# Optimization experiments

Hardware: AMD Instinct MI355X
Metric: run time of the kernel (lower is better)

The kernel has to match this reference:

```python
import jax, jax.numpy as jnp
import numpy as np
import math

C, NH, HD, L, P, FFN = 256, 8, 32, 1, 4, 512
H_BEV, W_BEV = 200, 100
NQ, BS, NV = 1000, 4, H_BEV * W_BEV
EPS = 1e-5


def _ln(x, g, b):
    m = x.mean(-1, keepdims=True)
    v = ((x - m) ** 2).mean(-1, keepdims=True)
    return (x - m) / jnp.sqrt(v + EPS) * g + b


def _mha(x, qpos, in_w, in_b, ow, ob):
    # nn.MultiheadAttention self-attention; key_pos = query_pos (shapes match)
    q = x + qpos
    k = x + qpos
    v = x
    wq, wk, wv = jnp.split(in_w, 3, axis=0)
    bq, bk, bv = jnp.split(in_b, 3, axis=0)
    bs, nq, _ = x.shape
    qh = (q @ wq.T + bq).reshape(bs, nq, NH, HD)
    kh = (k @ wk.T + bk).reshape(bs, nq, NH, HD)
    vh = (v @ wv.T + bv).reshape(bs, nq, NH, HD)
    scores = jnp.einsum('bqhd,bkhd->bhqk', qh, kh) / jnp.sqrt(jnp.float32(HD))
    attn = jax.nn.softmax(scores, axis=-1)
    out = jnp.einsum('bhqk,bkhd->bqhd', attn, vh).reshape(bs, nq, C)
    return out @ ow.T + ob


def _msdeform(x, qpos, value, ref, spatial_shapes, so_w, so_b, aw_w, aw_b, vp_w, vp_b, op_w, op_b):
    # Multi-scale deformable attention (single level), bilinear sampling with
    # align_corners=False convention and zero padding, as in the CUDA kernel.
    bs, nq, _ = x.shape
    q = x + qpos
    v = (value @ vp_w.T + vp_b).reshape(bs, NV, NH, HD).transpose(0, 2, 1, 3)  # [bs,nh,nv,hd]
    off = (q @ so_w.T + so_b).reshape(bs, nq, NH, L, P, 2)
    aw = jax.nn.softmax((q @ aw_w.T + aw_b).reshape(bs, nq, NH, L * P), axis=-1)
    aw = aw.reshape(bs, nq, NH, L, P)
    norm = jnp.stack([spatial_shapes[:, 1], spatial_shapes[:, 0]], -1).astype(jnp.float32)  # [L,2] = (W,H)
    loc = ref[:, :, None, :, None, :] + off / norm[None, None, None, :, None, :]  # [bs,nq,nh,L,P,2]
    loc = loc[:, :, :, 0]  # single level -> [bs,nq,nh,P,2]
    awp = aw[:, :, :, 0]   # [bs,nq,nh,P]
    x_im = loc[..., 0] * W_BEV - 0.5
    y_im = loc[..., 1] * H_BEV - 0.5
    x0 = jnp.floor(x_im)
    y0 = jnp.floor(y_im)
    lx = x_im - x0
    ly = y_im - y0
    x0i = x0.astype(jnp.int32)
    y0i = y0.astype(jnp.int32)
    acc = jnp.zeros((bs, NH, nq, P, HD), jnp.float32)
    for dy in (0, 1):
        for dx in (0, 1):
            xi = x0i + dx
            yi = y0i + dy
            w = (lx if dx else 1.0 - lx) * (ly if dy else 1.0 - ly)  # [bs,nq,nh,P]
            ok = ((xi >= 0) & (xi < W_BEV) & (yi >= 0) & (yi < H_BEV)).astype(jnp.float32)
            idx = jnp.clip(yi, 0, H_BEV - 1) * W_BEV + jnp.clip(xi, 0, W_BEV - 1)
            idx_t = idx.transpose(0, 2, 1, 3).reshape(bs, NH, nq * P)
            g = jnp.take_along_axis(v, idx_t[..., None], axis=2).reshape(bs, NH, nq, P, HD)
            acc = acc + g * (w * ok).transpose(0, 2, 1, 3)[..., None]
    out = (acc * awp.transpose(0, 2, 1, 3)[..., None]).sum(3)  # [bs,nh,nq,hd]
    out = out.transpose(0, 2, 1, 3).reshape(bs, nq, C)
    return out @ op_w.T + op_b


def setup_inputs() -> dict:
    key = jax.random.key(0)
    ks = jax.random.split(key, 24)
    f32 = jnp.float32

    def w(k, shp):
        fan = shp[-1]
        return (jax.random.normal(k, shp, f32) * (1.0 / np.sqrt(fan))).astype(f32)

    # sampling_offsets bias per _reset_parameters (radial grid init)
    thetas = np.arange(NH, dtype=np.float32) * (2.0 * math.pi / NH)
    grid = np.stack([np.cos(thetas), np.sin(thetas)], -1)
    grid = grid / np.abs(grid).max(-1, keepdims=True)
    grid = np.tile(grid[:, None, None, :], (1, L, P, 1))
    for i in range(P):
        grid[:, :, i, :] *= i + 1
    so_b = jnp.asarray(grid.reshape(-1), f32)

    return {
        'query': jax.random.normal(ks[0], (NQ, BS, C), f32),
        'value': jax.random.normal(ks[1], (NV, BS, C), f32),
        'query_pos': jax.random.normal(ks[2], (NQ, BS, C), f32),
        'reference_points': jax.random.uniform(ks[3], (BS, NQ, L, 2), f32),
        'spatial_shapes': jnp.array([[H_BEV, W_BEV]], jnp.int32),
        'level_start_index': jnp.zeros((L,), jnp.int32),
        'in_proj_w': w(ks[4], (3 * C, C)),
        'in_proj_b': jnp.zeros((3 * C,), f32),
        'mha_ow': w(ks[5], (C, C)),
        'mha_ob': jnp.zeros((C,), f32),
        'so_w': w(ks[6], (NH * L * P * 2, C)) * 0.01,
        'so_b': so_b,
        'aw_w': w(ks[7], (NH * L * P, C)) * 0.01,
        'aw_b': jnp.zeros((NH * L * P,), f32),
        'vp_w': w(ks[8], (C, C)),
        'vp_b': jnp.zeros((C,), f32),
        'op_w': w(ks[9], (C, C)),
        'op_b': jnp.zeros((C,), f32),
        'ffn_w1': w(ks[10], (FFN, C)),
        'ffn_b1': jnp.zeros((FFN,), f32),
        'ffn_w2': w(ks[11], (C, FFN)),
        'ffn_b2': jnp.zeros((C,), f32),
        'ln1_g': jnp.ones((C,), f32), 'ln1_b': jnp.zeros((C,), f32),
        'ln2_g': jnp.ones((C,), f32), 'ln2_b': jnp.zeros((C,), f32),
        'ln3_g': jnp.ones((C,), f32), 'ln3_b': jnp.zeros((C,), f32),
    }


def reference(query, value, query_pos, reference_points, spatial_shapes, level_start_index,
              in_proj_w, in_proj_b, mha_ow, mha_ob, so_w, so_b, aw_w, aw_b,
              vp_w, vp_b, op_w, op_b, ffn_w1, ffn_b1, ffn_w2, ffn_b2,
              ln1_g, ln1_b, ln2_g, ln2_b, ln3_g, ln3_b):
    # batch_first=False: (seq, bs, C) -> (bs, seq, C)
    x = query.transpose(1, 0, 2)
    val = value.transpose(1, 0, 2)
    qpos = query_pos.transpose(1, 0, 2)
    # self_attn -> norm (residual inside attn wrapper; dropout=0 in eval)
    x = _ln(x + _mha(x, qpos, in_proj_w, in_proj_b, mha_ow, mha_ob), ln1_g, ln1_b)
    # cross_attn (MSDeformAttn) -> norm
    x = _ln(x + _msdeform(x, qpos, val, reference_points, spatial_shapes,
                          so_w, so_b, aw_w, aw_b, vp_w, vp_b, op_w, op_b), ln2_g, ln2_b)
    # ffn -> norm
    h = jax.nn.relu(x @ ffn_w1.T + ffn_b1) @ ffn_w2.T + ffn_b2
    x = _ln(x + h, ln3_g, ln3_b)
    return x.transpose(1, 0, 2)
```

## Files before the change

kernel.cpp:

```cpp
#include <hip/hip_runtime.h>
#include <hip/hip_bf16.h>
#include <cmath>

#define BS   4
#define NQ   1000
#define CDIM 256
#define NH   8
#define HD   32
#define NVAL 20000
#define FFND 512
#define PN   4
#define WBEV 100
#define HBEV 200
#define TK   64

typedef __bf16 v8bf __attribute__((ext_vector_type(8)));
typedef __bf16 v2bf __attribute__((ext_vector_type(2)));
typedef float  v4f  __attribute__((ext_vector_type(4)));

__device__ __forceinline__ void gload_lds16(const void* g, void* l) {
    __builtin_amdgcn_global_load_lds(
        (const __attribute__((address_space(1))) unsigned int*)g,
        (__attribute__((address_space(3))) unsigned int*)l, 16, 0, 0);
}

__device__ __forceinline__ void vgemm64_block(
    int vb, const float* __restrict__ value, const __bf16* __restrict__ Wv,
    const float* __restrict__ bv, __bf16* __restrict__ vpj, char* smem)
{
    __bf16* As = (__bf16*)smem;
    __bf16* Bs = (__bf16*)(smem + 8192);
    int tid = threadIdx.x;
    int wave = tid >> 6, lane = tid & 63, quad = lane >> 4, n16 = lane & 15;
    int bm = vb * 64;
    int wm = (wave & 1) * 32, wn = (wave >> 1) * 128;
    v4f acc[2][8] = {};

    for (int k0 = 0; k0 < 256; k0 += 64) {
        float4 fa[2][2];
        #pragma unroll
        for (int i = 0; i < 2; i++) {
            int e = i * 256 + tid;
            int r = e >> 3, c = (e & 7) ^ (r & 7);
            const float* p = value + (long)(bm + r) * 256 + k0 + c * 8;
            fa[i][0] = *(const float4*)p;
            fa[i][1] = *(const float4*)(p + 4);
        }
        __syncthreads();
        #pragma unroll
        for (int i = 0; i < 2; i++) {
            int e = i * 256 + tid;
            v8bf v;
            v[0] = (__bf16)fa[i][0].x; v[1] = (__bf16)fa[i][0].y;
            v[2] = (__bf16)fa[i][0].z; v[3] = (__bf16)fa[i][0].w;
            v[4] = (__bf16)fa[i][1].x; v[5] = (__bf16)fa[i][1].y;
            v[6] = (__bf16)fa[i][1].z; v[7] = (__bf16)fa[i][1].w;
            *(v8bf*)(As + e * 8) = v;
        }
        #pragma unroll
        for (int i = 0; i < 8; i++) {
            int e = i * 256 + tid;
            int r = e >> 3, c = (e & 7) ^ (r & 7);
            gload_lds16(Wv + (long)r * 256 + k0 + c * 8, Bs + e * 8);
        }
        __syncthreads();
        #pragma unroll
        for (int s = 0; s < 2; s++) {
            v8bf af[2], bfr[8];
            #pragma unroll
            for (int mi = 0; mi < 2; mi++) {
                int row = wm + mi * 16 + n16;
                af[mi] = *(v8bf*)&As[row * 64 + (((quad + s * 4) ^ (row & 7))) * 8];
            }
            #pragma unroll
            for (int nj = 0; nj < 8; nj++) {
                int row = wn + nj * 16 + n16;
                bfr[nj] = *(v8bf*)&Bs[row * 64 + (((quad + s * 4) ^ (row & 7))) * 8];
            }
            #pragma unroll
            for (int mi = 0; mi < 2; mi++)
                #pragma unroll
                for (int nj = 0; nj < 8; nj++)
                    acc[mi][nj] = __builtin_amdgcn_mfma_f32_16x16x32_bf16(af[mi], bfr[nj], acc[mi][nj], 0, 0, 0);
        }
    }
    #pragma unroll
    for (int mi = 0; mi < 2; mi++) {
        #pragma unroll
        for (int r = 0; r < 4; r++) {
            int m = bm + wm + mi * 16 + quad * 4 + r;
            #pragma unroll
            for (int nj = 0; nj < 8; nj++) {
                int nn = wn + nj * 16 + n16;
                vpj[(long)m * 256 + nn] = (__bf16)(acc[mi][nj][r] + bv[nn]);
            }
        }
    }
}

__global__ __launch_bounds__(256) void prep_all_kernel(
    const float* __restrict__ query, const float* __restrict__ qpos,
    const float* __restrict__ in_w, const float* __restrict__ mha_ow,
    const float* __restrict__ vp_w, const float* __restrict__ op_w,
    const float* __restrict__ ffn_w1, const float* __restrict__ ffn_w2,
    const float* __restrict__ so_w, const float* __restrict__ aw_w,
    const float* __restrict__ so_b, const float* __restrict__ aw_b,
    float* __restrict__ x, float* __restrict__ qpos_t,
    __bf16* __restrict__ x_bf, __bf16* __restrict__ xq_bf,
    __bf16* __restrict__ wb, __bf16* __restrict__ wsmall,
    float* __restrict__ bsmall)
{
    int blk = blockIdx.x, tid = threadIdx.x;
    if (blk < 640) {
        long e = ((long)blk * 256 + tid) * 4;
        const float* src; long off;
        if      (e < 196608) { src = in_w;   off = e; }
        else if (e < 262144) { src = mha_ow; off = e - 196608; }
        else if (e < 327680) { src = vp_w;   off = e - 262144; }
        else if (e < 393216) { src = op_w;   off = e - 327680; }
        else if (e < 524288) { src = ffn_w1; off = e - 393216; }
        else                 { src = ffn_w2; off = e - 524288; }
        float4 v = *(const float4*)(src + off);
        __bf16* d = wb + e;
        d[0] = (__bf16)v.x; d[1] = (__bf16)v.y; d[2] = (__bf16)v.z; d[3] = (__bf16)v.w;
    } else if (blk < 4640) {
        int qb = blk - 640;
        int q = qb / BS, b = qb % BS;
        float qv = query[(q * BS + b) * CDIM + tid];
        float pv = qpos [(q * BS + b) * CDIM + tid];
        int o = (b * NQ + q) * CDIM + tid;
        x[o] = qv; qpos_t[o] = pv;
        x_bf[o] = (__bf16)qv; xq_bf[o] = (__bf16)(qv + pv);
    } else if (blk < 4672) {
        long e = ((long)(blk - 4640) * 256 + tid) * 4;
        int row = (int)(e >> 8), col = (int)(e & 255);
        float4 v = {0.f, 0.f, 0.f, 0.f};
        if (row < 64)      v = *(const float4*)(so_w + row * 256 + col);
        else if (row < 96) v = *(const float4*)(aw_w + (row - 64) * 256 + col);
        __bf16* d = wsmall + e;
        d[0] = (__bf16)v.x; d[1] = (__bf16)v.y; d[2] = (__bf16)v.z; d[3] = (__bf16)v.w;
    } else {
        if (tid < 128) bsmall[tid] = tid < 64 ? so_b[tid] : (tid < 96 ? aw_b[tid - 64] : 0.f);
    }
}

__global__ __launch_bounds__(256) void qkvv_kernel(
    const __bf16* __restrict__ xq, const __bf16* __restrict__ xv,
    const __bf16* __restrict__ W, const float* __restrict__ bias,
    __bf16* __restrict__ qk, __bf16* __restrict__ vh,
    const float* __restrict__ value, const __bf16* __restrict__ Wv,
    const float* __restrict__ bv, __bf16* __restrict__ vpj, int voff)
{
    __shared__ __align__(16) char smem[40960];
    int tid = threadIdx.x;
    if ((int)blockIdx.x >= 756) {
        vgemm64_block(blockIdx.x - 756 + voff, value, Wv, bv, vpj, smem);
        return;
    }
    int blk = blockIdx.x;
    int bn = (blk % 12) * 64, bm = (blk / 12) * 64;
    __bf16* As = (__bf16*)smem;
    __bf16* Bs = (__bf16*)(smem + 8192);
    const __bf16* A = (bn < 512) ? xq : xv;
    int wave = tid >> 6, lane = tid & 63, quad = lane >> 4, n16 = lane & 15;
    int wm = (wave & 1) * 32, wn = (wave >> 1) * 32;
    v4f acc[2][2] = {};

    for (int k0 = 0; k0 < 256; k0 += 64) {
        __syncthreads();
        #pragma unroll
        for (int i = 0; i < 2; i++) {
            int e = i * 256 + tid;
            int r = e >> 3, c = (e & 7) ^ (r & 7);
            int row = bm + r; if (row > BS * NQ - 1) row = BS * NQ - 1;
            gload_lds16(A + (long)row * 256 + k0 + c * 8, As + e * 8);
        }
        #pragma unroll
        for (int i = 0; i < 2; i++) {
            int e = i * 256 + tid;
            int r = e >> 3, c = (e & 7) ^ (r & 7);
            gload_lds16(W + (long)(bn + r) * 256 + k0 + c * 8, Bs + e * 8);
        }
        __syncthreads();
        #pragma unroll
        for (int s = 0; s < 2; s++) {
            v8bf af[2], bfr[2];
            #pragma unroll
            for (int mi = 0; mi < 2; mi++) {
                int row = wm + mi * 16 + n16;
                af[mi] = *(v8bf*)&As[row * 64 + (((quad + s * 4) ^ (row & 7))) * 8];
            }
            #pragma unroll
            for (int nj = 0; nj < 2; nj++) {
                int row = wn + nj * 16 + n16;
                bfr[nj] = *(v8bf*)&Bs[row * 64 + (((quad + s * 4) ^ (row & 7))) * 8];
            }
            #pragma unroll
            for (int mi = 0; mi < 2; mi++)
                #pragma unroll
                for (int nj = 0; nj < 2; nj++)
                    acc[mi][nj] = __builtin_amdgcn_mfma_f32_16x16x32_bf16(af[mi], bfr[nj], acc[mi][nj], 0, 0, 0);
        }
    }

    #pragma unroll
    for (int mi = 0; mi < 2; mi++) {
        #pragma unroll
        for (int r = 0; r < 4; r++) {
            int m = bm + wm + mi * 16 + quad * 4 + r;
            if (m >= BS * NQ) continue;
            #pragma unroll
            for (int nj = 0; nj < 2; nj++) {
                int nn = bn + wn + nj * 16 + n16;
                float v = acc[mi][nj][r] + bias[nn];
                if (nn < 512) qk[(long)m * 512 + nn] = (__bf16)v;
                else          vh[(long)m * 256 + (nn - 512)] = (__bf16)v;
            }
        }
    }
}

__global__ __launch_bounds__(256) void fattnv_kernel(
    const __bf16* __restrict__ qk, const __bf16* __restrict__ vh,
    __bf16* __restrict__ aout,
    const float* __restrict__ value, const __bf16* __restrict__ Wv,
    const float* __restrict__ bv, __bf16* __restrict__ vpj, int voff)
{
    __shared__ __align__(16) char smem[40960];
    int tid = threadIdx.x;
    if ((int)blockIdx.x >= 512) {
        vgemm64_block(blockIdx.x - 512 + voff, value, Wv, bv, vpj, smem);
        return;
    }
    int fb = blockIdx.x;
    int qt = fb & 15, h = (fb >> 4) & 7, b = fb >> 7;
    __bf16* Ks = (__bf16*)smem;
    __bf16* Vt = (__bf16*)(smem + 10240);
    __bf16* Pl = (__bf16*)(smem + 19456);
    int wave = tid >> 6, lane = tid & 63, quad = lane >> 4, n = lane & 15;
    int q0 = qt * 64 + wave * 16;
    const float scale = 0.17677669529663687f;
    const float M0 = 8.0f;

    int qrow = q0 + n; if (qrow > NQ - 1) qrow = NQ - 1;
    v8bf aq = *(const v8bf*)(qk + (long)(b * NQ + qrow) * 512 + h * HD + quad * 8);

    v4f o0 = {}, o1 = {};
    float lp[4] = {0.f, 0.f, 0.f, 0.f};

    int sv = tid >> 7;
    int t2 = tid & 127;
    int key = t2 & 63;
    int d16 = (t2 >> 6) * 16;

    v8bf stg0, stg1;
    auto loadtile = [&](int k0) {
        int krow = k0 + key; if (krow > NQ - 1) krow = NQ - 1;
        const __bf16* p = sv ? (vh + (long)(b * NQ + krow) * CDIM + h * HD + d16)
                             : (qk + (long)(b * NQ + krow) * 512 + 256 + h * HD + d16);
        stg0 = *(const v8bf*)p;
        stg1 = *(const v8bf*)(p + 8);
    };

    loadtile(0);
    int pb = 0;
    for (int k0 = 0; k0 < NQ; k0 += TK) {
        if (sv == 0) {
            *(v8bf*)&Ks[(pb * 64 + key) * 40 + d16]     = stg0;
            *(v8bf*)&Ks[(pb * 64 + key) * 40 + d16 + 8] = stg1;
        } else {
            #pragma unroll
            for (int j = 0; j < 8; j++) {
                Vt[(pb * 32 + d16 + j) * 72 + key]            = stg0[j];
                Vt[(pb * 32 + d16 + 8 + j) * 72 + (key ^ 16)] = stg1[j];
            }
        }
        if (k0 + TK < NQ) loadtile(k0 + TK);
        __syncthreads();

        v8bf bk0 = *(v8bf*)&Ks[(pb * 64 +      n) * 40 + quad * 8];
        v8bf bk1 = *(v8bf*)&Ks[(pb * 64 + 16 + n) * 40 + quad * 8];
        v8bf bk2 = *(v8bf*)&Ks[(pb * 64 + 32 + n) * 40 + quad * 8];
        v8bf bk3 = *(v8bf*)&Ks[(pb * 64 + 48 + n) * 40 + quad * 8];
        v4f z = {};
        v4f S0 = __builtin_amdgcn_mfma_f32_16x16x32_bf16(aq, bk0, z, 0, 0, 0);
        v4f S1 = __builtin_amdgcn_mfma_f32_16x16x32_bf16(aq, bk1, z, 0, 0, 0);
        v4f S2 = __builtin_amdgcn_mfma_f32_16x16x32_bf16(aq, bk2, z, 0, 0, 0);
        v4f S3 = __builtin_amdgcn_mfma_f32_16x16x32_bf16(aq, bk3, z, 0, 0, 0);

        bool last = (k0 + TK > NQ);
        float p0[4], p1[4], p2[4], p3[4];
        #pragma unroll
        for (int r = 0; r < 4; r++) {
            p0[r] = __expf(fmaf(S0[r], scale, -M0));
            p1[r] = __expf(fmaf(S1[r], scale, -M0));
            p2[r] = __expf(fmaf(S2[r], scale, -M0));
            p3[r] = __expf(fmaf(S3[r], scale, -M0));
            if (last) {
                if (k0 + 32 + n >= NQ) p2[r] = 0.f;
                if (k0 + 48 + n >= NQ) p3[r] = 0.f;
            }
            lp[r] += p0[r] + p1[r] + p2[r] + p3[r];
        }
        #pragma unroll
        for (int r = 0; r < 4; r++) {
            __bf16* pp = &Pl[(wave * 16 + quad * 4 + r) * 72];
            pp[n]      = (__bf16)p0[r];
            pp[16 + n] = (__bf16)p1[r];
            pp[32 + n] = (__bf16)p2[r];
            pp[48 + n] = (__bf16)p3[r];
        }
        asm volatile("s_waitcnt lgkmcnt(0)" ::: "memory");
        v8bf ap0 = *(v8bf*)&Pl[(wave * 16 + n) * 72 + quad * 8];
        v8bf ap1 = *(v8bf*)&Pl[(wave * 16 + n) * 72 + 32 + quad * 8];
        int swz = ((n >> 3) & 1) << 4;
        int c0 = (quad * 8) ^ swz;
        int c1 = (32 + quad * 8) ^ swz;
        v8bf bv00 = *(v8bf*)&Vt[(pb * 32 +      n) * 72 + c0];
        v8bf bv01 = *(v8bf*)&Vt[(pb * 32 +      n) * 72 + c1];
        v8bf bv10 = *(v8bf*)&Vt[(pb * 32 + 16 + n) * 72 + c0];
        v8bf bv11 = *(v8bf*)&Vt[(pb * 32 + 16 + n) * 72 + c1];
        o0 = __builtin_amdgcn_mfma_f32_16x16x32_bf16(ap0, bv00, o0, 0, 0, 0);
        o0 = __builtin_amdgcn_mfma_f32_16x16x32_bf16(ap1, bv01, o0, 0, 0, 0);
        o1 = __builtin_amdgcn_mfma_f32_16x16x32_bf16(ap0, bv10, o1, 0, 0, 0);
        o1 = __builtin_amdgcn_mfma_f32_16x16x32_bf16(ap1, bv11, o1, 0, 0, 0);
        pb ^= 1;
    }

    #pragma unroll
    for (int r = 0; r < 4; r++) {
        float l = lp[r];
        #pragma unroll
        for (int off = 1; off < 16; off <<= 1) l += __shfl_xor(l, off, 16);
        int q = q0 + quad * 4 + r;
        if (q < NQ) {
            float invl = 1.0f / l;
            __bf16* op = aout + ((long)(b * NQ + q) * CDIM + h * HD);
            op[n]      = (__bf16)(o0[r] * invl);
            op[16 + n] = (__bf16)(o1[r] * invl);
        }
    }
}

__global__ __launch_bounds__(256) void gln1s_kernel(
    const __bf16* __restrict__ A, const __bf16* __restrict__ W,
    const float* __restrict__ bias, const float* __restrict__ res,
    const float* __restrict__ g, const float* __restrict__ beta,
    const float* __restrict__ qpos_t,
    const __bf16* __restrict__ Wsm, const float* __restrict__ bsm,
    float* __restrict__ outf, float* __restrict__ soawO,
    const float* __restrict__ value, const __bf16* __restrict__ Wv,
    const float* __restrict__ bv, __bf16* __restrict__ vpj, int voff)
{
    __shared__ __align__(16) char smem[43776];
    int tid = threadIdx.x;
    if ((int)blockIdx.x >= 250) {
        vgemm64_block(blockIdx.x - 250 + voff, value, Wv, bv, vpj, smem);
        return;
    }
    __bf16* As  = (__bf16*)smem;
    __bf16* Bs  = (__bf16*)(smem + 2048);
    __bf16* Axq = (__bf16*)(smem + 34816);
    float* redS = (float*)(smem + 43264);
    float* redQ = redS + 64;
    int bm = blockIdx.x * 16;
    int wave = tid >> 6, lane = tid & 63, quad = lane >> 4, n16 = lane & 15;
    int wn = wave * 64;
    v4f acc[4] = {};

    for (int k0 = 0; k0 < 256; k0 += 64) {
        __syncthreads();
        if (tid < 128) {
            int e = tid;
            int r = e >> 3, c = (e & 7) ^ (r & 7);
            gload_lds16(A + (long)(bm + r) * 256 + k0 + c * 8, As + e * 8);
        }
        #pragma unroll
        for (int i = 0; i < 8; i++) {
            int e = i * 256 + tid;
            int r = e >> 3, c = (e & 7) ^ (r & 7);
            gload_lds16(W + (long)r * 256 + k0 + c * 8, Bs + e * 8);
        }
        __syncthreads();
        #pragma unroll
        for (int s = 0; s < 2; s++) {
            v8bf af = *(v8bf*)&As[n16 * 64 + (((quad + s * 4) ^ (n16 & 7))) * 8];
            #pragma unroll
            for (int nj = 0; nj < 4; nj++) {
                int row = wn + nj * 16 + n16;
                v8bf bfr = *(v8bf*)&Bs[row * 64 + (((quad + s * 4) ^ (row & 7))) * 8];
                acc[nj] = __builtin_amdgcn_mfma_f32_16x16x32_bf16(af, bfr, acc[nj], 0, 0, 0);
            }
        }
    }

    float y[4][4], s1[4] = {}, s2[4] = {};
    #pragma unroll
    for (int r = 0; r < 4; r++) {
        int m = bm + quad * 4 + r;
        #pragma unroll
        for (int nj = 0; nj < 4; nj++) {
            int nn = wn + nj * 16 + n16;
            float v = acc[nj][r] + bias[nn] + res[(long)m * 256 + nn];
            y[r][nj] = v;
            s1[r] += v; s2[r] += v * v;
        }
    }
    #pragma unroll
    for (int r = 0; r < 4; r++) {
        #pragma unroll
        for (int off = 1; off < 16; off <<= 1) {
            s1[r] += __shfl_xor(s1[r], off, 16);
            s2[r] += __shfl_xor(s2[r], off, 16);
        }
    }
    if (n16 == 0) {
        #pragma unroll
        for (int r = 0; r < 4; r++) {
            redS[wave * 16 + quad * 4 + r] = s1[r];
            redQ[wave * 16 + quad * 4 + r] = s2[r];
        }
    }
    __syncthreads();
    #pragma unroll
    for (int r = 0; r < 4; r++) {
        int mr = quad * 4 + r;
        float ts = redS[mr] + redS[16 + mr] + redS[32 + mr] + redS[48 + mr];
        float tq = redQ[mr] + redQ[16 + mr] + redQ[32 + mr] + redQ[48 + mr];
        float mean = ts * (1.0f / 256.0f);
        float var = tq * (1.0f / 256.0f) - mean * mean;
        float rinv = rsqrtf(var + 1e-5f);
        int m = bm + mr;
        #pragma unroll
        for (int nj = 0; nj < 4; nj++) {
            int nn = wn + nj * 16 + n16;
            float o = (y[r][nj] - mean) * rinv * g[nn] + beta[nn];
            outf[(long)m * 256 + nn] = o;
            Axq[mr * 264 + nn] = (__bf16)(o + qpos_t[(long)m * 256 + nn]);
        }
    }
    __syncthreads();
    if (wave < 3) {
        v4f sacc[2] = {};
        #pragma unroll
        for (int k0 = 0; k0 < 256; k0 += 32) {
            v8bf af = *(v8bf*)&Axq[n16 * 264 + k0 + quad * 8];
            #pragma unroll
            for (int t = 0; t < 2; t++) {
                int col = wave * 32 + t * 16 + n16;
                v8bf bw = *(const v8bf*)(Wsm + (long)col * 256 + k0 + quad * 8);
                sacc[t] = __builtin_amdgcn_mfma_f32_16x16x32_bf16(af, bw, sacc[t], 0, 0, 0);
            }
        }
        #pragma unroll
        for (int t = 0; t < 2; t++)
            #pragma unroll
            for (int r = 0; r < 4; r++) {
                int mm = bm + quad * 4 + r;
                int col = wave * 32 + t * 16 + n16;
                soawO[(long)mm * 96 + col] = sacc[t][r] + bsm[col];
            }
    }
}

__global__ __launch_bounds__(256) void msds_kernel(
    const __bf16* __restrict__ vproj, const float* __restrict__ soaw,
    const float* __restrict__ refp, __bf16* __restrict__ out)
{
    int t = threadIdx.x;
    int bq = blockIdx.x * 2 + (t >> 7);
    int b = bq / NQ; int q = bq % NQ;
    int t2 = t & 127;
    int h = t2 >> 4;
    int d0 = (t2 & 15) * 2;
    float rx = refp[(b * NQ + q) * 2 + 0];
    float ry = refp[(b * NQ + q) * 2 + 1];
    const float* rowp = soaw + (long)(b * NQ + q) * 96;
    const float* offp = rowp + h * 8;
    const float* awp  = rowp + 64 + h * 4;
    float a0 = awp[0], a1 = awp[1], a2 = awp[2], a3 = awp[3];
    float m = fmaxf(fmaxf(a0, a1), fmaxf(a2, a3));
    float e0 = __expf(a0 - m), e1 = __expf(a1 - m), e2 = __expf(a2 - m), e3 = __expf(a3 - m);
    float invs = 1.0f / (e0 + e1 + e2 + e3);
    float accA = 0.f, accB = 0.f;
    #pragma unroll
    for (int p = 0; p < PN; p++) {
        float ew = (p == 0 ? e0 : p == 1 ? e1 : p == 2 ? e2 : e3) * invs;
        float xim = rx * (float)WBEV + offp[p * 2 + 0] - 0.5f;
        float yim = ry * (float)HBEV + offp[p * 2 + 1] - 0.5f;
        float x0f = floorf(xim), y0f = floorf(yim);
        float lx = xim - x0f, ly = yim - y0f;
        int x0 = (int)x0f, y0 = (int)y0f;
        float gA = 0.f, gB = 0.f;
        #pragma unroll
        for (int dy = 0; dy < 2; dy++) {
            #pragma unroll
            for (int dx = 0; dx < 2; dx++) {
                int xi = x0 + dx, yi = y0 + dy;
                float w = (dx ? lx : 1.f - lx) * (dy ? ly : 1.f - ly);
                bool ok = (xi >= 0 && xi < WBEV && yi >= 0 && yi < HBEV);
                int xc = min(max(xi, 0), WBEV - 1);
                int yc = min(max(yi, 0), HBEV - 1);
                int idx = yc * WBEV + xc;
                v2bf gv = *(const v2bf*)(vproj + ((long)(idx * BS + b)) * CDIM + h * HD + d0);
                float wk = (ok ? w : 0.f);
                gA += wk * (float)gv[0];
                gB += wk * (float)gv[1];
            }
        }
        accA += ew * gA;
        accB += ew * gB;
    }
    v2bf o2; o2[0] = (__bf16)accA; o2[1] = (__bf16)accB;
    *(v2bf*)(out + (long)(b * NQ + q) * CDIM + h * HD + d0) = o2;
}

__global__ __launch_bounds__(256) void gtail_kernel(
    const __bf16* __restrict__ A, const __bf16* __restrict__ Wop,
    const float* __restrict__ opb, const float* __restrict__ res,
    const float* __restrict__ g2, const float* __restrict__ b2ln,
    const __bf16* __restrict__ W1, const float* __restrict__ b1,
    const __bf16* __restrict__ W2, const float* __restrict__ bff2,
    const float* __restrict__ g3, const float* __restrict__ b3ln,
    float* __restrict__ outf)
{
    __shared__ __align__(16) char smem[59904];
    __bf16* As  = (__bf16*)smem;
    __bf16* Bs  = (__bf16*)(smem + 2048);
    __bf16* As2 = (__bf16*)(smem + 34816);
    __bf16* h1s = (__bf16*)(smem + 43008);
    float* redS = (float*)(smem + 59392);
    float* redQ = (float*)(smem + 59648);
    int tid = threadIdx.x;
    int bm = blockIdx.x * 16;
    int wave = tid >> 6, lane = tid & 63, quad = lane >> 4, n16 = lane & 15;
    int wn = wave * 64;

    v4f acc[4] = {};
    for (int k0 = 0; k0 < 256; k0 += 64) {
        __syncthreads();
        if (tid < 128) {
            int e = tid;
            int r = e >> 3, c = (e & 7) ^ (r & 7);
            gload_lds16(A + (long)(bm + r) * 256 + k0 + c * 8, As + e * 8);
        }
        #pragma unroll
        for (int i = 0; i < 8; i++) {
            int e = i * 256 + tid;
            int r = e >> 3, c = (e & 7) ^ (r & 7);
            gload_lds16(Wop + (long)r * 256 + k0 + c * 8, Bs + e * 8);
        }
        __syncthreads();
        #pragma unroll
        for (int s = 0; s < 2; s++) {
            v8bf af = *(v8bf*)&As[n16 * 64 + (((quad + s * 4) ^ (n16 & 7))) * 8];
            #pragma unroll
            for (int nj = 0; nj < 4; nj++) {
                int row = wn + nj * 16 + n16;
                v8bf bfr = *(v8bf*)&Bs[row * 64 + (((quad + s * 4) ^ (row & 7))) * 8];
                acc[nj] = __builtin_amdgcn_mfma_f32_16x16x32_bf16(af, bfr, acc[nj], 0, 0, 0);
            }
        }
    }
    float yv[4][4], s1[4] = {}, s2[4] = {};
    #pragma unroll
    for (int r = 0; r < 4; r++) {
        int m = bm + quad * 4 + r;
        #pragma unroll
        for (int nj = 0; nj < 4; nj++) {
            int nn = wn + nj * 16 + n16;
            float v = acc[nj][r] + opb[nn] + res[(long)m * 256 + nn];
            yv[r][nj] = v;
            s1[r] += v; s2[r] += v * v;
        }
    }
    #pragma unroll
    for (int r = 0; r < 4; r++) {
        #pragma unroll
        for (int off = 1; off < 16; off <<= 1) {
            s1[r] += __shfl_xor(s1[r], off, 16);
            s2[r] += __shfl_xor(s2[r], off, 16);
        }
    }
    if (n16 == 0) {
        #pragma unroll
        for (int r = 0; r < 4; r++) {
            redS[wave * 16 + quad * 4 + r] = s1[r];
            redQ[wave * 16 + quad * 4 + r] = s2[r];
        }
    }
    __syncthreads();
    #pragma unroll
    for (int r = 0; r < 4; r++) {
        int mr = quad * 4 + r;
        float ts = redS[mr] + redS[16 + mr] + redS[32 + mr] + redS[48 + mr];
        float tq = redQ[mr] + redQ[16 + mr] + redQ[32 + mr] + redQ[48 + mr];
        float mean = ts * (1.0f / 256.0f);
        float var = tq * (1.0f / 256.0f) - mean * mean;
        float rinv = rsqrtf(var + 1e-5f);
        #pragma unroll
        for (int nj = 0; nj < 4; nj++) {
            int nn = wn + nj * 16 + n16;
            float o = (yv[r][nj] - mean) * rinv * g2[nn] + b2ln[nn];
            yv[r][nj] = o;
            int c = nn & 63;
            As2[wave * 1024 + mr * 64 + ((((c >> 3)) ^ (mr & 7)) << 3) + (c & 7)] = (__bf16)o;
        }
    }

    #pragma unroll 1
    for (int H = 0; H < 2; H++) {
        v4f accB[4] = {};
        for (int k0 = 0; k0 < 256; k0 += 64) {
            __syncthreads();
            #pragma unroll
            for (int i = 0; i < 8; i++) {
                int e = i * 256 + tid;
                int r = e >> 3, c = (e & 7) ^ (r & 7);
                gload_lds16(W1 + (long)(H * 256 + r) * 256 + k0 + c * 8, Bs + e * 8);
            }
            __syncthreads();
            int kc = k0 >> 6;
            #pragma unroll
            for (int s = 0; s < 2; s++) {
                v8bf af = *(v8bf*)&As2[kc * 1024 + n16 * 64 + (((quad + s * 4) ^ (n16 & 7))) * 8];
                #pragma unroll
                for (int nj = 0; nj < 4; nj++) {
                    int row = wn + nj * 16 + n16;
                    v8bf bfr = *(v8bf*)&Bs[row * 64 + (((quad + s * 4) ^ (row & 7))) * 8];
                    accB[nj] = __builtin_amdgcn_mfma_f32_16x16x32_bf16(af, bfr, accB[nj], 0, 0, 0);
                }
            }
        }
        #pragma unroll
        for (int r = 0; r < 4; r++) {
            int mr = quad * 4 + r;
            #pragma unroll
            for (int nj = 0; nj < 4; nj++) {
                int col = H * 256 + wn + nj * 16 + n16;
                float v = accB[nj][r] + b1[col];
                v = fmaxf(v, 0.f);
                int kc = col >> 6, c = col & 63;
                h1s[kc * 1024 + mr * 64 + ((((c >> 3)) ^ (mr & 7)) << 3) + (c & 7)] = (__bf16)v;
            }
        }
    }

    v4f acc3[4] = {};
    for (int k0 = 0; k0 < 512; k0 += 64) {
        __syncthreads();
        #pragma unroll
        for (int i = 0; i < 8; i++) {
            int e = i * 256 + tid;
            int r = e >> 3, c = (e & 7) ^ (r & 7);
            gload_lds16(W2 + (long)r * 512 + k0 + c * 8, Bs + e * 8);
        }
        __syncthreads();
        int kc = k0 >> 6;
        #pragma unroll
        for (int s = 0; s < 2; s++) {
            v8bf af = *(v8bf*)&h1s[kc * 1024 + n16 * 64 + (((quad + s * 4) ^ (n16 & 7))) * 8];
            #pragma unroll
            for (int nj = 0; nj < 4; nj++) {
                int row = wn + nj * 16 + n16;
                v8bf bfr = *(v8bf*)&Bs[row * 64 + (((quad + s * 4) ^ (row & 7))) * 8];
                acc3[nj] = __builtin_amdgcn_mfma_f32_16x16x32_bf16(af, bfr, acc3[nj], 0, 0, 0);
            }
        }
    }
    float y3[4][4], t1[4] = {}, t2[4] = {};
    #pragma unroll
    for (int r = 0; r < 4; r++) {
        #pragma unroll
        for (int nj = 0; nj < 4; nj++) {
            int nn = wn + nj * 16 + n16;
            float v = acc3[nj][r] + bff2[nn] + yv[r][nj];
            y3[r][nj] = v;
            t1[r] += v; t2[r] += v * v;
        }
    }
    #pragma unroll
    for (int r = 0; r < 4; r++) {
        #pragma unroll
        for (int off = 1; off < 16; off <<= 1) {
            t1[r] += __shfl_xor(t1[r], off, 16);
            t2[r] += __shfl_xor(t2[r], off, 16);
        }
    }
    __syncthreads();
    if (n16 == 0) {
        #pragma unroll
        for (int r = 0; r < 4; r++) {
            redS[wave * 16 + quad * 4 + r] = t1[r];
            redQ[wave * 16 + quad * 4 + r] = t2[r];
        }
    }
    __syncthreads();
    #pragma unroll
    for (int r = 0; r < 4; r++) {
        int mr = quad * 4 + r;
        float ts = redS[mr] + redS[16 + mr] + redS[32 + mr] + redS[48 + mr];
        float tq = redQ[mr] + redQ[16 + mr] + redQ[32 + mr] + redQ[48 + mr];
        float mean = ts * (1.0f / 256.0f);
        float var = tq * (1.0f / 256.0f) - mean * mean;
        float rinv = rsqrtf(var + 1e-5f);
        int m = bm + mr;
        int b = m / NQ, q = m - b * NQ;
        #pragma unroll
        for (int nj = 0; nj < 4; nj++) {
            int nn = wn + nj * 16 + n16;
            float o = (y3[r][nj] - mean) * rinv * g3[nn] + b3ln[nn];
            outf[(long)(q * BS + b) * 256 + nn] = o;
        }
    }
}

extern "C" void kernel_launch(void* const* d_in, const int* in_sizes, int n_in,
                              void* d_out, int out_size, void* d_ws, size_t ws_size,
                              hipStream_t stream) {
    const float* query = (const float*)d_in[0];
    const float* value = (const float*)d_in[1];
    const float* qpos  = (const float*)d_in[2];
    const float* refp  = (const float*)d_in[3];
    const float* in_w  = (const float*)d_in[6];
    const float* in_b  = (const float*)d_in[7];
    const float* mha_ow = (const float*)d_in[8];
    const float* mha_ob = (const float*)d_in[9];
    const float* so_w  = (const float*)d_in[10];
    const float* so_b  = (const float*)d_in[11];
    const float* aw_w  = (const float*)d_in[12];
    const float* aw_b  = (const float*)d_in[13];
    const float* vp_w  = (const float*)d_in[14];
    const float* vp_b  = (const float*)d_in[15];
    const float* op_w  = (const float*)d_in[16];
    const float* op_b  = (const float*)d_in[17];
    const float* ffn_w1 = (const float*)d_in[18];
    const float* ffn_b1 = (const float*)d_in[19];
    const float* ffn_w2 = (const float*)d_in[20];
    const float* ffn_b2 = (const float*)d_in[21];
    const float* ln1_g = (const float*)d_in[22];
    const float* ln1_b = (const float*)d_in[23];
    const float* ln2_g = (const float*)d_in[24];
    const float* ln2_b = (const float*)d_in[25];
    const float* ln3_g = (const float*)d_in[26];
    const float* ln3_b = (const float*)d_in[27];
    float* out = (float*)d_out;

    const long NTOK = (long)BS * NQ * CDIM;

    float* x      = (float*)d_ws;
    float* qpos_t = x + NTOK;
    float* x1     = qpos_t + NTOK;
    float* x2     = x1 + NTOK;
    float* soaw   = x2 + NTOK;
    float* bsmall = soaw + (long)BS * NQ * 96;
    __bf16* x_bf   = (__bf16*)(bsmall + 128);
    __bf16* xq_bf  = x_bf + NTOK;
    __bf16* qk_bf  = xq_bf + NTOK;
    __bf16* vh_bf  = qk_bf + 2 * NTOK;
    __bf16* aA_bf  = vh_bf + NTOK;
    __bf16* x2_bf  = aA_bf + NTOK;
    __bf16* h1_bf  = x2_bf + NTOK;
    __bf16* vpj_bf = h1_bf + 2 * NTOK;
    __bf16* wb     = vpj_bf + (long)BS * NVAL * CDIM;
    __bf16* inw_b  = wb;
    __bf16* mow_b  = wb + 196608;
    __bf16* vpw_b  = wb + 262144;
    __bf16* opw_b  = wb + 327680;
    __bf16* fw1_b  = wb + 393216;
    __bf16* fw2_b  = wb + 524288;
    __bf16* wsmall = wb + 655360;

    dim3 blk(256);

    prep_all_kernel<<<4673, blk, 0, stream>>>(
        query, qpos, in_w, mha_ow, vp_w, op_w, ffn_w1, ffn_w2,
        so_w, aw_w, so_b, aw_b,
        x, qpos_t, x_bf, xq_bf, wb, wsmall, bsmall);

    qkvv_kernel<<<1173, blk, 0, stream>>>(xq_bf, x_bf, inw_b, in_b, qk_bf, vh_bf,
                                          value, vpw_b, vp_b, vpj_bf, 0);

    fattnv_kernel<<<929, blk, 0, stream>>>(qk_bf, vh_bf, aA_bf,
                                           value, vpw_b, vp_b, vpj_bf, 417);

    gln1s_kernel<<<666, blk, 0, stream>>>(
        aA_bf, mow_b, mha_ob, x, ln1_g, ln1_b, qpos_t, wsmall, bsmall,
        x1, soaw, value, vpw_b, vp_b, vpj_bf, 834);

    msds_kernel<<<2000, blk, 0, stream>>>(vpj_bf, soaw, refp, aA_bf);

    gtail_kernel<<<250, blk, 0, stream>>>(
        aA_bf, opw_b, op_b, x1, ln2_g, ln2_b,
        fw1_b, ffn_b1, fw2_b, ffn_b2, ln3_g, ln3_b, out);
}
```

Before: 270.5 us.

## Split value projection into standalone kernel and widen FFN tail blocks to 512 threads

Before this change, the value-projection GEMM blocks were spread across the qkv, attention and LN1 kernels to overlap with them. They now run as one dedicated vgemm kernel with 1250 blocks, and the host kernels shrink their LDS to match their own needs. Separately, the FFN tail kernel goes to 512 threads (8 waves, each covering 32 columns), which gives more parallelism per 16-row block in its 250-block grid. The cost is losing the overlap of the value GEMM with the latency-bound attention work, plus one extra launch.

```diff
diff --git a/kernel.cpp b/kernel.cpp
--- a/kernel.cpp
+++ b/kernel.cpp
@@ -24,15 +24,16 @@
         (__attribute__((address_space(3))) unsigned int*)l, 16, 0, 0);
 }
 
-__device__ __forceinline__ void vgemm64_block(
-    int vb, const float* __restrict__ value, const __bf16* __restrict__ Wv,
-    const float* __restrict__ bv, __bf16* __restrict__ vpj, char* smem)
+__global__ __launch_bounds__(256) void vgemm_kernel(
+    const float* __restrict__ value, const __bf16* __restrict__ Wv,
+    const float* __restrict__ bv, __bf16* __restrict__ vpj)
 {
+    __shared__ __align__(16) char smem[40960];
     __bf16* As = (__bf16*)smem;
     __bf16* Bs = (__bf16*)(smem + 8192);
     int tid = threadIdx.x;
     int wave = tid >> 6, lane = tid & 63, quad = lane >> 4, n16 = lane & 15;
-    int bm = vb * 64;
+    int bm = blockIdx.x * 64;
     int wm = (wave & 1) * 32, wn = (wave >> 1) * 128;
     v4f acc[2][8] = {};
 
@@ -147,16 +148,10 @@
 __global__ __launch_bounds__(256) void qkvv_kernel(
     const __bf16* __restrict__ xq, const __bf16* __restrict__ xv,
     const __bf16* __restrict__ W, const float* __restrict__ bias,
-    __bf16* __restrict__ qk, __bf16* __restrict__ vh,
-    const float* __restrict__ value, const __bf16* __restrict__ Wv,
-    const float* __restrict__ bv, __bf16* __restrict__ vpj, int voff)
+    __bf16* __restrict__ qk, __bf16* __restrict__ vh)
 {
-    __shared__ __align__(16) char smem[40960];
+    __shared__ __align__(16) char smem[16384];
     int tid = threadIdx.x;
-    if ((int)blockIdx.x >= 756) {
-        vgemm64_block(blockIdx.x - 756 + voff, value, Wv, bv, vpj, smem);
-        return;
-    }
     int blk = blockIdx.x;
     int bn = (blk % 12) * 64, bm = (blk / 12) * 64;
     __bf16* As = (__bf16*)smem;
@@ -222,16 +217,10 @@
 
 __global__ __launch_bounds__(256) void fattnv_kernel(
     const __bf16* __restrict__ qk, const __bf16* __restrict__ vh,
-    __bf16* __restrict__ aout,
-    const float* __restrict__ value, const __bf16* __restrict__ Wv,
-    const float* __restrict__ bv, __bf16* __restrict__ vpj, int voff)
+    __bf16* __restrict__ aout)
 {
-    __shared__ __align__(16) char smem[40960];
+    __shared__ __align__(16) char smem[28672];
     int tid = threadIdx.x;
-    if ((int)blockIdx.x >= 512) {
-        vgemm64_block(blockIdx.x - 512 + voff, value, Wv, bv, vpj, smem);
-        return;
-    }
     int fb = blockIdx.x;
     int qt = fb & 15, h = (fb >> 4) & 7, b = fb >> 7;
     __bf16* Ks = (__bf16*)smem;
@@ -348,16 +337,10 @@
     const float* __restrict__ g, const float* __restrict__ beta,
     const float* __restrict__ qpos_t,
     const __bf16* __restrict__ Wsm, const float* __restrict__ bsm,
-    float* __restrict__ outf, float* __restrict__ soawO,
-    const float* __restrict__ value, const __bf16* __restrict__ Wv,
-    const float* __restrict__ bv, __bf16* __restrict__ vpj, int voff)
+    float* __restrict__ outf, float* __restrict__ soawO)
 {
     __shared__ __align__(16) char smem[43776];
     int tid = threadIdx.x;
-    if ((int)blockIdx.x >= 250) {
-        vgemm64_block(blockIdx.x - 250 + voff, value, Wv, bv, vpj, smem);
-        return;
-    }
     __bf16* As  = (__bf16*)smem;
     __bf16* Bs  = (__bf16*)(smem + 2048);
     __bf16* Axq = (__bf16*)(smem + 34816);
@@ -515,7 +498,7 @@
     *(v2bf*)(out + (long)(b * NQ + q) * CDIM + h * HD + d0) = o2;
 }
 
-__global__ __launch_bounds__(256) void gtail_kernel(
+__global__ __launch_bounds__(512) void gtail_kernel(
     const __bf16* __restrict__ A, const __bf16* __restrict__ Wop,
     const float* __restrict__ opb, const float* __restrict__ res,
     const float* __restrict__ g2, const float* __restrict__ b2ln,
@@ -524,19 +507,20 @@
     const float* __restrict__ g3, const float* __restrict__ b3ln,
     float* __restrict__ outf)
 {
-    __shared__ __align__(16) char smem[59904];
+    __shared__ __align__(16) char smem[60416];
     __bf16* As  = (__bf16*)smem;
     __bf16* Bs  = (__bf16*)(smem + 2048);
     __bf16* As2 = (__bf16*)(smem + 34816);
     __bf16* h1s = (__bf16*)(smem + 43008);
     float* redS = (float*)(smem + 59392);
-    float* redQ = (float*)(smem + 59648);
+    float* redQ = (float*)(smem + 59904);
     int tid = threadIdx.x;
     int bm = blockIdx.x * 16;
     int wave = tid >> 6, lane = tid & 63, quad = lane >> 4, n16 = lane & 15;
-    int wn = wave * 64;
-
-    v4f acc[4] = {};
+    int wn = wave * 32;
+    int mr_ = quad * 4;
+
+    v4f acc[2] = {};
     for (int k0 = 0; k0 < 256; k0 += 64) {
         __syncthreads();
         if (tid < 128) {
@@ -545,8 +529,8 @@
             gload_lds16(A + (long)(bm + r) * 256 + k0 + c * 8, As + e * 8);
         }
         #pragma unroll
-        for (int i = 0; i < 8; i++) {
-            int e = i * 256 + tid;
+        for (int i = 0; i < 4; i++) {
+            int e = i * 512 + tid;
             int r = e >> 3, c = (e & 7) ^ (r & 7);
             gload_lds16(Wop + (long)r * 256 + k0 + c * 8, Bs + e * 8);
         }
@@ -555,19 +539,19 @@
         for (int s = 0; s < 2; s++) {
             v8bf af = *(v8bf*)&As[n16 * 64 + (((quad + s * 4) ^ (n16 & 7))) * 8];
             #pragma unroll
-            for (int nj = 0; nj < 4; nj++) {
+            for (int nj = 0; nj < 2; nj++) {
                 int row = wn + nj * 16 + n16;
                 v8bf bfr = *(v8bf*)&Bs[row * 64 + (((quad + s * 4) ^ (row & 7))) * 8];
                 acc[nj] = __builtin_amdgcn_mfma_f32_16x16x32_bf16(af, bfr, acc[nj], 0, 0, 0);
             }
         }
     }
-    float yv[4][4], s1[4] = {}, s2[4] = {};
-    #pragma unroll
-    for (int r = 0; r < 4; r++) {
-        int m = bm + quad * 4 + r;
-        #pragma unroll
-        for (int nj = 0; nj < 4; nj++) {
+    float yv[4][2], s1[4] = {}, s2[4] = {};
+    #pragma unroll
+    for (int r = 0; r < 4; r++) {
+        int m = bm + mr_ + r;
+        #pragma unroll
+        for (int nj = 0; nj < 2; nj++) {
             int nn = wn + nj * 16 + n16;
             float v = acc[nj][r] + opb[nn] + res[(long)m * 256 + nn];
             yv[r][nj] = v;
@@ -585,37 +569,38 @@
     if (n16 == 0) {
         #pragma unroll
         for (int r = 0; r < 4; r++) {
-            redS[wave * 16 + quad * 4 + r] = s1[r];
-            redQ[wave * 16 + quad * 4 + r] = s2[r];
+            redS[wave * 16 + mr_ + r] = s1[r];
+            redQ[wave * 16 + mr_ + r] = s2[r];
         }
     }
     __syncthreads();
     #pragma unroll
     for (int r = 0; r < 4; r++) {
-        int mr = quad * 4 + r;
-        float ts = redS[mr] + redS[16 + mr] + redS[32 + mr] + redS[48 + mr];
-        float tq = redQ[mr] + redQ[16 + mr] + redQ[32 + mr] + redQ[48 + mr];
+        int mr = mr_ + r;
+        float ts = 0.f, tq = 0.f;
+        #pragma unroll
+        for (int j = 0; j < 8; j++) { ts += redS[j * 16 + mr]; tq += redQ[j * 16 + mr]; }
         float mean = ts * (1.0f / 256.0f);
         float var = tq * (1.0f / 256.0f) - mean * mean;
         float rinv = rsqrtf(var + 1e-5f);
         #pragma unroll
-        for (int nj = 0; nj < 4; nj++) {
+        for (int nj = 0; nj < 2; nj++) {
             int nn = wn + nj * 16 + n16;
             float o = (yv[r][nj] - mean) * rinv * g2[nn] + b2ln[nn];
             yv[r][nj] = o;
-            int c = nn & 63;
-            As2[wave * 1024 + mr * 64 + ((((c >> 3)) ^ (mr & 7)) << 3) + (c & 7)] = (__bf16)o;
+            int kc = nn >> 6, c6 = nn & 63;
+            As2[kc * 1024 + mr * 64 + (((c6 >> 3) ^ (mr & 7)) << 3) + (c6 & 7)] = (__bf16)o;
         }
     }
 
     #pragma unroll 1
     for (int H = 0; H < 2; H++) {
-        v4f accB[4] = {};
+        v4f accB[2] = {};
         for (int k0 = 0; k0 < 256; k0 += 64) {
             __syncthreads();
             #pragma unroll
-            for (int i = 0; i < 8; i++) {
-                int e = i * 256 + tid;
+            for (int i = 0; i < 4; i++) {
+                int e = i * 512 + tid;
                 int r = e >> 3, c = (e & 7) ^ (r & 7);
                 gload_lds16(W1 + (long)(H * 256 + r) * 256 + k0 + c * 8, Bs + e * 8);
             }
@@ -625,7 +610,7 @@
             for (int s = 0; s < 2; s++) {
                 v8bf af = *(v8bf*)&As2[kc * 1024 + n16 * 64 + (((quad + s * 4) ^ (n16 & 7))) * 8];
                 #pragma unroll
-                for (int nj = 0; nj < 4; nj++) {
+                for (int nj = 0; nj < 2; nj++) {
                     int row = wn + nj * 16 + n16;
                     v8bf bfr = *(v8bf*)&Bs[row * 64 + (((quad + s * 4) ^ (row & 7))) * 8];
                     accB[nj] = __builtin_amdgcn_mfma_f32_16x16x32_bf16(af, bfr, accB[nj], 0, 0, 0);
@@ -634,24 +619,24 @@
         }
         #pragma unroll
         for (int r = 0; r < 4; r++) {
-            int mr = quad * 4 + r;
-            #pragma unroll
-            for (int nj = 0; nj < 4; nj++) {
+            int mr = mr_ + r;
+            #pragma unroll
+            for (int nj = 0; nj < 2; nj++) {
                 int col = H * 256 + wn + nj * 16 + n16;
                 float v = accB[nj][r] + b1[col];
                 v = fmaxf(v, 0.f);
-                int kc = col >> 6, c = col & 63;
-                h1s[kc * 1024 + mr * 64 + ((((c >> 3)) ^ (mr & 7)) << 3) + (c & 7)] = (__bf16)v;
-            }
-        }
-    }
-
-    v4f acc3[4] = {};
+                int kc = col >> 6, c6 = col & 63;
+                h1s[kc * 1024 + mr * 64 + (((c6 >> 3) ^ (mr & 7)) << 3) + (c6 & 7)] = (__bf16)v;
+            }
+        }
+    }
+
+    v4f acc3[2] = {};
     for (int k0 = 0; k0 < 512; k0 += 64) {
         __syncthreads();
         #pragma unroll
-        for (int i = 0; i < 8; i++) {
-            int e = i * 256 + tid;
+        for (int i = 0; i < 4; i++) {
+            int e = i * 512 + tid;
             int r = e >> 3, c = (e & 7) ^ (r & 7);
             gload_lds16(W2 + (long)r * 512 + k0 + c * 8, Bs + e * 8);
         }
@@ -661,18 +646,18 @@
         for (int s = 0; s < 2; s++) {
             v8bf af = *(v8bf*)&h1s[kc * 1024 + n16 * 64 + (((quad + s * 4) ^ (n16 & 7))) * 8];
             #pragma unroll
-            for (int nj = 0; nj < 4; nj++) {
+            for (int nj = 0; nj < 2; nj++) {
                 int row = wn + nj * 16 + n16;
                 v8bf bfr = *(v8bf*)&Bs[row * 64 + (((quad + s * 4) ^ (row & 7))) * 8];
                 acc3[nj] = __builtin_amdgcn_mfma_f32_16x16x32_bf16(af, bfr, acc3[nj], 0, 0, 0);
             }
         }
     }
-    float y3[4][4], t1[4] = {}, t2[4] = {};
-    #pragma unroll
-    for (int r = 0; r < 4; r++) {
-        #pragma unroll
-        for (int nj = 0; nj < 4; nj++) {
+    float y3[4][2], t1[4] = {}, t2[4] = {};
+    #pragma unroll
+    for (int r = 0; r < 4; r++) {
+        #pragma unroll
+        for (int nj = 0; nj < 2; nj++) {
             int nn = wn + nj * 16 + n16;
             float v = acc3[nj][r] + bff2[nn] + yv[r][nj];
             y3[r][nj] = v;
@@ -691,23 +676,24 @@
     if (n16 == 0) {
         #pragma unroll
         for (int r = 0; r < 4; r++) {
-            redS[wave * 16 + quad * 4 + r] = t1[r];
-            redQ[wave * 16 + quad * 4 + r] = t2[r];
+            redS[wave * 16 + mr_ + r] = t1[r];
+            redQ[wave * 16 + mr_ + r] = t2[r];
         }
     }
     __syncthreads();
     #pragma unroll
     for (int r = 0; r < 4; r++) {
-        int mr = quad * 4 + r;
-        float ts = redS[mr] + redS[16 + mr] + redS[32 + mr] + redS[48 + mr];
-        float tq = redQ[mr] + redQ[16 + mr] + redQ[32 + mr] + redQ[48 + mr];
+        int mr = mr_ + r;
+        float ts = 0.f, tq = 0.f;
+        #pragma unroll
+        for (int j = 0; j < 8; j++) { ts += redS[j * 16 + mr]; tq += redQ[j * 16 + mr]; }
         float mean = ts * (1.0f / 256.0f);
         float var = tq * (1.0f / 256.0f) - mean * mean;
         float rinv = rsqrtf(var + 1e-5f);
         int m = bm + mr;
         int b = m / NQ, q = m - b * NQ;
         #pragma unroll
-        for (int nj = 0; nj < 4; nj++) {
+        for (int nj = 0; nj < 2; nj++) {
             int nn = wn + nj * 16 + n16;
             float o = (y3[r][nj] - mean) * rinv * g3[nn] + b3ln[nn];
             outf[(long)(q * BS + b) * 256 + nn] = o;
@@ -778,19 +764,19 @@
         so_w, aw_w, so_b, aw_b,
         x, qpos_t, x_bf, xq_bf, wb, wsmall, bsmall);
 
-    qkvv_kernel<<<1173, blk, 0, stream>>>(xq_bf, x_bf, inw_b, in_b, qk_bf, vh_bf,
-                                          value, vpw_b, vp_b, vpj_bf, 0);
-
-    fattnv_kernel<<<929, blk, 0, stream>>>(qk_bf, vh_bf, aA_bf,
-                                           value, vpw_b, vp_b, vpj_bf, 417);
-
-    gln1s_kernel<<<666, blk, 0, stream>>>(
+    qkvv_kernel<<<756, blk, 0, stream>>>(xq_bf, x_bf, inw_b, in_b, qk_bf, vh_bf);
+
+    vgemm_kernel<<<1250, blk, 0, stream>>>(value, vpw_b, vp_b, vpj_bf);
+
+    fattnv_kernel<<<512, blk, 0, stream>>>(qk_bf, vh_bf, aA_bf);
+
+    gln1s_kernel<<<250, blk, 0, stream>>>(
         aA_bf, mow_b, mha_ob, x, ln1_g, ln1_b, qpos_t, wsmall, bsmall,
-        x1, soaw, value, vpw_b, vp_b, vpj_bf, 834);
+        x1, soaw);
 
     msds_kernel<<<2000, blk, 0, stream>>>(vpj_bf, soaw, refp, aA_bf);
 
-    gtail_kernel<<<250, blk, 0, stream>>>(
+    gtail_kernel<<<250, dim3(512), 0, stream>>>(
         aA_bf, opw_b, op_b, x1, ln2_g, ln2_b,
         fw1_b, ffn_b1, fw2_b, ffn_b2, ln3_g, ln3_b, out);
 }
```

Result: faster. 264.3 us (-2.3%).
